# Optimization experiments

Measured on AMD Instinct MI355X. Metric: run time of the kernel, lower is better.

## Reference

```python
import jax, jax.numpy as jnp
import numpy as np

RADIUS = 8
NUM = 200
EPS = 1e-8


def _conv2d(x, k, pad_mode):
    # x: [B,1,H,W], k: [kh,kw]; same-size conv with given numpy-style padding mode
    ph, pw = k.shape[0] // 2, k.shape[1] // 2
    xp = jnp.pad(x, ((0, 0), (0, 0), (ph, ph), (pw, pw)), mode=pad_mode)
    return jax.lax.conv_general_dilated(
        xp, k[None, None], (1, 1), 'VALID',
        dimension_numbers=('NCHW', 'OIHW', 'NCHW'))


def _gauss_kernel7():
    xs = np.arange(7, dtype=np.float32) - 3.0
    g = np.exp(-0.5 * xs ** 2)
    g /= g.sum()
    return jnp.asarray(np.outer(g, g))


def get_corners(imgs):
    B, _, H, W = imgs.shape
    # kornia rgb_to_grayscale
    gray = 0.299 * imgs[:, 0:1] + 0.587 * imgs[:, 1:2] + 0.114 * imgs[:, 2:3]
    # kornia CornerGFTT: sobel gradients (normalized), gaussian-smoothed structure tensor, min eigenvalue
    sob = jnp.array([[-1., 0., 1.], [-2., 0., 2.], [-1., 0., 1.]], jnp.float32) / 8.0
    dx = _conv2d(gray, sob, 'edge')
    dy = _conv2d(gray, sob.T, 'edge')
    g = _gauss_kernel7()
    dx2 = _conv2d(dx * dx, g, 'reflect')
    dy2 = _conv2d(dy * dy, g, 'reflect')
    dxy = _conv2d(dx * dy, g, 'reflect')
    tr = dx2 + dy2
    det = dx2 * dy2 - dxy * dxy
    resp = 0.5 * (tr - jnp.sqrt(jnp.abs(tr * tr - 4.0 * det)))  # GFTT score (min eigval)
    # kornia nms2d with 5x5 window: keep local maxima
    mp = jax.lax.reduce_window(resp, -jnp.inf, jax.lax.max,
                               (1, 1, 5, 5), (1, 1, 1, 1),
                               [(0, 0), (0, 0), (2, 2), (2, 2)])
    resp = jnp.where(resp == mp, resp, 0.0)
    # unfold/mask/fold with kernel=stride=RADIUS == per non-overlapping 8x8 block:
    # keep elements equal to the block max and > 0
    r = RADIUS
    blk = resp.reshape(B, 1, H // r, r, W // r, r)
    bmax = blk.max(axis=(3, 5), keepdims=True)
    blk = jnp.where((blk > 0) & (blk == bmax), blk, 0.0)
    corners = blk.reshape(B, H * W)
    # top-200 scatter then binarize
    vals, idx = jax.lax.top_k(corners, NUM)
    out = jnp.zeros_like(corners).at[jnp.arange(B)[:, None], idx].set(vals)
    return (out > 0).astype(imgs.dtype).reshape(B, 1, H, W)


def setup_inputs() -> dict:
    key = jax.random.key(0)
    k1, k2, k3, k4 = jax.random.split(key, 4)
    B, N, D, H, W = 16, 2048, 256, 384, 384
    return {
        'descriptors': jax.random.normal(k1, (B, N, D), jnp.float32),
        'scores': jax.random.uniform(k2, (B, N), jnp.float32),
        'scores_dense': jax.random.normal(k3, (B, 1, H, W), jnp.float32),
        'imgs': jax.random.uniform(k4, (B, 3, H, W), jnp.float32),
    }


def reference(descriptors, scores, scores_dense, imgs):
    corners = get_corners(imgs)
    # all-pairs cosine similarity within each batch: pcos[b,i,j]
    norms = jnp.linalg.norm(descriptors, axis=-1)  # [B,N]
    dots = jnp.einsum('bnd,bmd->bnm', descriptors, descriptors)
    pcos = dots / jnp.maximum(norms[:, :, None] * norms[:, None, :], EPS)
    # BCEWithLogitsLoss(scores_dense, corners), mean reduction
    bce = jnp.mean(jnp.logaddexp(0.0, scores_dense) - scores_dense * corners)
    return bce + jnp.mean(jax.nn.relu(pcos))
```

## Files before the change

kernel.cpp:

```cpp
#include <hip/hip_runtime.h>

#define H 384
#define W 384
#define HWSZ (H * W)
#define NB 16
#define ND 2048
#define DD 256

#define OFF_RESP  256
#define OFF_CVAL  9437440
#define OFF_CPOS  9584896
#define OFF_DESCB 9732352
#define OFF_INV   26509568
#define OFF_PSOFT 26640640
#define OFF_PGEMM 26643200
#define OFF_PCORN 26652160

__device__ __forceinline__ int clampi(int v) { return v < 0 ? 0 : (v > 383 ? 383 : v); }
__device__ __forceinline__ int refl(int v) { return v < 0 ? -v : (v >= 384 ? 766 - v : v); }

__device__ __forceinline__ unsigned f2e4m3(float x) {
  float a = fabsf(x);
  unsigned s = (__float_as_uint(x) >> 31) << 7;
  if (a >= 448.f) return s | 0x7E;
  if (a < 0.015625f) {
    int m = (int)rintf(a * 512.f);
    return s | (unsigned)m;
  }
  unsigned u = __float_as_uint(a);
  u += 0x7FFFF + ((u >> 20) & 1);
  unsigned e = (u >> 23) - 120;
  unsigned m = (u >> 20) & 7;
  return s | (e << 3) | m;
}

typedef float f32x4 __attribute__((ext_vector_type(4)));

__device__ __forceinline__ void load_lds16(const void* g, void* l) {
  __builtin_amdgcn_global_load_lds((const __attribute__((address_space(1))) void*)g,
                                   (__attribute__((address_space(3))) void*)l, 16, 0, 0);
}

__global__ __launch_bounds__(256) void stage1_kernel(const float* __restrict__ imgs,
                                                     float* __restrict__ resp,
                                                     const float* __restrict__ desc,
                                                     unsigned char* __restrict__ descF8,
                                                     float* __restrict__ invn) {
  __shared__ float pbuf[4448];
  __shared__ float ubuf[3648];
  float* p0 = pbuf;
  float* p1 = pbuf + 1482;
  float* p2 = pbuf + 2964;
  float* glf = ubuf;
  float* t0 = ubuf;
  float* t1 = ubuf + 1216;
  float* t2 = ubuf + 2432;

  if (blockIdx.x >= 2304) {
    int wave = threadIdx.x >> 6, lane = threadIdx.x & 63;
    int row = (blockIdx.x - 2304) * 4 + wave;
    const float4* src = (const float4*)(desc + (size_t)row * DD);
    float4 v = src[lane];
    unsigned pk = f2e4m3(v.x) | (f2e4m3(v.y) << 8) | (f2e4m3(v.z) << 16) | (f2e4m3(v.w) << 24);
    ((unsigned*)(descF8 + (size_t)row * DD))[lane] = pk;
    float ss = v.x * v.x + v.y * v.y + v.z * v.z + v.w * v.w;
    for (int off = 32; off; off >>= 1) ss += __shfl_down(ss, off, 64);
    if (lane == 0) invn[row] = 1.f / fmaxf(sqrtf(ss), 1e-4f);
    return;
  }

  const float GW[7] = {0.0044330482f, 0.0540055826f, 0.2420362294f, 0.3990502160f,
                       0.2420362294f, 0.0540055826f, 0.0044330482f};
  int bid = blockIdx.x;
  int b = bid / 144;
  int t = bid % 144;
  int Y0 = (t / 12) * 32, X0 = (t % 12) * 32;
  const float* ib = imgs + (size_t)b * 3 * HWSZ;

  for (int i = threadIdx.x; i < 1600; i += 256) {
    int r = i / 40, c = i % 40;
    int gy = clampi(Y0 - 4 + r), gx = clampi(X0 - 4 + c);
    const float* p = ib + gy * W + gx;
    glf[r * 41 + c] = 0.299f * p[0] + 0.587f * p[HWSZ] + 0.114f * p[2 * HWSZ];
  }
  __syncthreads();

  bool interior = (X0 >= 32 && X0 <= 320 && Y0 >= 32 && Y0 <= 320);

  if (interior) {
    for (int i = threadIdx.x; i < 1444; i += 256) {
      int r = i / 38, c = i % 38;
      const float* g0 = glf + r * 41 + c;
      float a = g0[0],  bb = g0[1],  cc = g0[2];
      float d = g0[41],              e = g0[43];
      float f = g0[82], g = g0[83],  h = g0[84];
      float dx = 0.125f * ((cc - a) + 2.f * (e - d) + (h - f));
      float dy = 0.125f * ((f - a) + 2.f * (g - bb) + (h - cc));
      p0[r * 39 + c] = dx * dx;
      p1[r * 39 + c] = dy * dy;
      p2[r * 39 + c] = dx * dy;
    }
  } else {
    for (int i = threadIdx.x; i < 1444; i += 256) {
      int r = i / 38, c = i % 38;
      int py = refl(Y0 - 3 + r), px = refl(X0 - 3 + c);
      int ym = clampi(py - 1) - (Y0 - 4), y0 = py - (Y0 - 4), yp = clampi(py + 1) - (Y0 - 4);
      int xm = clampi(px - 1) - (X0 - 4), x0 = px - (X0 - 4), xp = clampi(px + 1) - (X0 - 4);
      float a = glf[ym * 41 + xm], bb = glf[ym * 41 + x0], cc = glf[ym * 41 + xp];
      float d = glf[y0 * 41 + xm], e = glf[y0 * 41 + xp];
      float f = glf[yp * 41 + xm], g = glf[yp * 41 + x0], h = glf[yp * 41 + xp];
      float dx = 0.125f * ((cc - a) + 2.f * (e - d) + (h - f));
      float dy = 0.125f * ((f - a) + 2.f * (g - bb) + (h - cc));
      p0[r * 39 + c] = dx * dx;
      p1[r * 39 + c] = dy * dy;
      p2[r * 39 + c] = dx * dy;
    }
  }
  __syncthreads();

  for (int g = threadIdx.x; g < 304; g += 256) {
    int r = g >> 3, c0 = (g & 7) * 4;
    {
      float a[10];
#pragma unroll
      for (int dc = 0; dc < 10; dc++) a[dc] = p0[r * 39 + c0 + dc];
#pragma unroll
      for (int k = 0; k < 4; k++) {
        float sv = 0.f;
#pragma unroll
        for (int j = 0; j < 7; j++) sv += GW[j] * a[k + j];
        t0[r * 32 + c0 + k] = sv;
      }
    }
    {
      float a[10];
#pragma unroll
      for (int dc = 0; dc < 10; dc++) a[dc] = p1[r * 39 + c0 + dc];
#pragma unroll
      for (int k = 0; k < 4; k++) {
        float sv = 0.f;
#pragma unroll
        for (int j = 0; j < 7; j++) sv += GW[j] * a[k + j];
        t1[r * 32 + c0 + k] = sv;
      }
    }
    {
      float a[10];
#pragma unroll
      for (int dc = 0; dc < 10; dc++) a[dc] = p2[r * 39 + c0 + dc];
#pragma unroll
      for (int k = 0; k < 4; k++) {
        float sv = 0.f;
#pragma unroll
        for (int j = 0; j < 7; j++) sv += GW[j] * a[k + j];
        t2[r * 32 + c0 + k] = sv;
      }
    }
  }
  __syncthreads();

  {
    int r0 = (threadIdx.x >> 5) * 4, c = threadIdx.x & 31;
    float s0[4], s1[4], s2[4];
    {
      float a[10];
#pragma unroll
      for (int dr = 0; dr < 10; dr++) a[dr] = t0[(r0 + dr) * 32 + c];
#pragma unroll
      for (int k = 0; k < 4; k++) {
        float sv = 0.f;
#pragma unroll
        for (int j = 0; j < 7; j++) sv += GW[j] * a[k + j];
        s0[k] = sv;
      }
    }
    {
      float a[10];
#pragma unroll
      for (int dr = 0; dr < 10; dr++) a[dr] = t1[(r0 + dr) * 32 + c];
#pragma unroll
      for (int k = 0; k < 4; k++) {
        float sv = 0.f;
#pragma unroll
        for (int j = 0; j < 7; j++) sv += GW[j] * a[k + j];
        s1[k] = sv;
      }
    }
    {
      float a[10];
#pragma unroll
      for (int dr = 0; dr < 10; dr++) a[dr] = t2[(r0 + dr) * 32 + c];
#pragma unroll
      for (int k = 0; k < 4; k++) {
        float sv = 0.f;
#pragma unroll
        for (int j = 0; j < 7; j++) sv += GW[j] * a[k + j];
        s2[k] = sv;
      }
    }
#pragma unroll
    for (int k = 0; k < 4; k++) {
      float tr = s0[k] + s1[k];
      float det = s0[k] * s1[k] - s2[k] * s2[k];
      float disc = tr * tr - 4.f * det;
      float rv = 0.5f * (tr - sqrtf(fabsf(disc)));
      resp[(size_t)b * HWSZ + (Y0 + r0 + k) * W + (X0 + c)] = rv;
    }
  }
}

__global__ __launch_bounds__(256) void stage2_kernel(const float* __restrict__ resp,
                                                     float* __restrict__ cval,
                                                     unsigned* __restrict__ cpos,
                                                     const float4* __restrict__ sd4,
                                                     float* __restrict__ psoft) {
  __shared__ float rl[68][37];
  __shared__ float rmx[68][32];
  __shared__ float r4[4];

  if (blockIdx.x >= 1152) {
    int sb = blockIdx.x - 1152;
    float s = 0.f;
    int base = sb * 256 + threadIdx.x;
#pragma unroll
    for (int it = 0; it < 4; it++) {
      float4 v = sd4[base + it * 147456];
      s += fmaxf(v.x, 0.f) + log1pf(expf(-fabsf(v.x))) +
           fmaxf(v.y, 0.f) + log1pf(expf(-fabsf(v.y))) +
           fmaxf(v.z, 0.f) + log1pf(expf(-fabsf(v.z))) +
           fmaxf(v.w, 0.f) + log1pf(expf(-fabsf(v.w)));
    }
    for (int off = 32; off; off >>= 1) s += __shfl_down(s, off, 64);
    if ((threadIdx.x & 63) == 0) r4[threadIdx.x >> 6] = s;
    __syncthreads();
    if (threadIdx.x == 0) psoft[sb] = r4[0] + r4[1] + r4[2] + r4[3];
    return;
  }

  int bid = blockIdx.x;
  int b = bid / 72;
  int t = bid % 72;
  int Y0 = (t / 12) * 64, X0 = (t % 12) * 32;
  const float* rb = resp + (size_t)b * HWSZ;

  for (int i = threadIdx.x; i < 68 * 36; i += 256) {
    int r = i / 36, c = i % 36;
    int gy = Y0 - 2 + r, gx = X0 - 2 + c;
    float v = -INFINITY;
    if (gy >= 0 && gy < H && gx >= 0 && gx < W) v = rb[gy * W + gx];
    rl[r][c] = v;
  }
  __syncthreads();

  for (int i = threadIdx.x; i < 68 * 32; i += 256) {
    int r = i / 32, c = i % 32;
    float m = rl[r][c];
    m = fmaxf(m, rl[r][c + 1]);
    m = fmaxf(m, rl[r][c + 2]);
    m = fmaxf(m, rl[r][c + 3]);
    m = fmaxf(m, rl[r][c + 4]);
    rmx[r][c] = m;
  }
  __syncthreads();

  for (int i = threadIdx.x; i < 2048; i += 256) {
    int r = i / 32, c = i % 32;
    float m = rmx[r][c];
    m = fmaxf(m, rmx[r + 1][c]);
    m = fmaxf(m, rmx[r + 2][c]);
    m = fmaxf(m, rmx[r + 3][c]);
    m = fmaxf(m, rmx[r + 4][c]);
    float v = rl[r + 2][c + 2];
    rl[r + 2][c + 2] = (v == m) ? v : 0.f;
  }
  __syncthreads();

  if (threadIdx.x < 32) {
    int bi = threadIdx.x >> 2, bj = threadIdx.x & 3;
    float bv = 0.f;
    unsigned bp = 0;
    for (int rr = 0; rr < 8; rr++)
      for (int cc = 0; cc < 8; cc++) {
        float v = rl[bi * 8 + rr + 2][bj * 8 + cc + 2];
        if (v > bv) { bv = v; bp = (unsigned)((Y0 + bi * 8 + rr) * W + (X0 + bj * 8 + cc)); }
      }
    int ci = b * 2304 + (Y0 / 8 + bi) * 48 + (X0 / 8 + bj);
    cval[ci] = bv;
    cpos[ci] = bp;
  }
}

__global__ __launch_bounds__(256) void stage3_kernel(const float* __restrict__ cval,
                                                     const unsigned* __restrict__ cpos,
                                                     const float* __restrict__ sd,
                                                     float* __restrict__ pcorn,
                                                     const unsigned char* __restrict__ descF8,
                                                     const float* __restrict__ invn,
                                                     float* __restrict__ pgemm) {
  alignas(16) __shared__ char smem[32768];
  int tid = threadIdx.x;

  if (blockIdx.x < 16) {
    int* hist = (int*)smem;
    int* pick = (int*)(smem + 1024);
    int* eqcnt = (int*)(smem + 1032);
    int* ri = (int*)(smem + 1040);
    unsigned* eqpos = (unsigned*)(smem + 1056);
    float* r4 = (float*)(smem + 2080);

    int b = blockIdx.x;
    int t = tid;
    int lane = t & 63;

    unsigned bits[9], pos[9];
#pragma unroll
    for (int q = 0; q < 9; q++) {
      int i = t + q * 256;
      unsigned vb = 0, p = 0;
      if (i < 2304) {
        float v = cval[b * 2304 + i];
        if (v > 0.f) { vb = __float_as_uint(v); p = cpos[b * 2304 + i]; }
      }
      bits[q] = vb; pos[q] = p;
    }

    int P = 0;
#pragma unroll
    for (int q = 0; q < 9; q++) P += (bits[q] != 0u);
    for (int off = 32; off; off >>= 1) P += __shfl_down(P, off, 64);
    if (lane == 0) ri[t >> 6] = P;
    __syncthreads();
    int Ptot = ri[0] + ri[1] + ri[2] + ri[3];
    if (Ptot == 0) { if (t == 0) pcorn[b] = 0.f; return; }
    int K = Ptot < 200 ? Ptot : 200;

    unsigned prefix = 0;
    int krem = K;
    for (int shift = 24; shift >= 0; shift -= 8) {
      hist[t] = 0;
      __syncthreads();
#pragma unroll
      for (int q = 0; q < 9; q++) {
        if (bits[q] != 0u &&
            (shift == 24 || (bits[q] >> (shift + 8)) == (prefix >> (shift + 8))))
          atomicAdd(&hist[(bits[q] >> shift) & 0xFF], 1);
      }
      __syncthreads();
      if (t < 64) {
        int h0 = hist[4 * t], h1 = hist[4 * t + 1], h2 = hist[4 * t + 2], h3 = hist[4 * t + 3];
        int tot = h0 + h1 + h2 + h3;
        int acc = tot;
        for (int d = 1; d < 64; d <<= 1) {
          int o = __shfl_down(acc, d, 64);
          if (t + d < 64) acc += o;
        }
        int excl = acc - tot;
        int G3 = excl, G2 = excl + h3, G1 = excl + h3 + h2, G0 = excl + h3 + h2 + h1;
        if (G0 < krem && G0 + h0 >= krem) { pick[0] = 4 * t;     pick[1] = G0; }
        if (G1 < krem && G1 + h1 >= krem) { pick[0] = 4 * t + 1; pick[1] = G1; }
        if (G2 < krem && G2 + h2 >= krem) { pick[0] = 4 * t + 2; pick[1] = G2; }
        if (G3 < krem && G3 + h3 >= krem) { pick[0] = 4 * t + 3; pick[1] = G3; }
      }
      __syncthreads();
      prefix |= ((unsigned)pick[0]) << shift;
      krem -= pick[1];
      __syncthreads();
    }

    if (t == 0) *eqcnt = 0;
    __syncthreads();
    float s = 0.f;
#pragma unroll
    for (int q = 0; q < 9; q++) {
      if (bits[q] > prefix) s += sd[(size_t)b * HWSZ + pos[q]];
      else if (bits[q] != 0u && bits[q] == prefix) {
        int idx = atomicAdd(eqcnt, 1);
        if (idx < 256) eqpos[idx] = pos[q];
      }
    }
    __syncthreads();
    int m = *eqcnt;
    if (m <= krem) {
      if (t < m) s += sd[(size_t)b * HWSZ + eqpos[t]];
    } else {
      int mm = m < 256 ? m : 256;
      if (t < mm) {
        unsigned p = eqpos[t];
        int rank = 0;
        for (int u = 0; u < mm; u++) rank += (eqpos[u] < p);
        if (rank < krem) s += sd[(size_t)b * HWSZ + p];
      }
    }
    for (int off = 32; off; off >>= 1) s += __shfl_down(s, off, 64);
    if (lane == 0) r4[t >> 6] = s;
    __syncthreads();
    if (t == 0) pcorn[b] = r4[0] + r4[1] + r4[2] + r4[3];
    return;
  }

  char* lA = smem;
  char* lB = smem + 16384;

  int bxl = blockIdx.x - 16;
  int bx = ((bxl & 7) * 272) + (bxl >> 3);
  int batch = bx / 136;
  int rem = bx % 136;
  int ti = 0, rowlen = 16;
  while (rem >= rowlen) { rem -= rowlen; rowlen--; ti++; }
  int tj = ti + rem;

  const unsigned char* Ab = descF8 + (size_t)batch * ND * DD;
  const float* inv = invn + batch * ND;
  int I0 = ti * 128, J0 = tj * 128;

  int wave = tid >> 6, lane = tid & 63;
  int rm = lane & 15, kq = lane >> 4;
  int wr = wave >> 1, wc = wave & 1;
  int lrow = lane >> 3;
  int lcolb = ((lane & 7) ^ lrow) << 4;
  int cx = rm & 7;

  f32x4 accf[4][4];
#pragma unroll
  for (int m = 0; m < 4; m++)
#pragma unroll
    for (int n = 0; n < 4; n++) accf[m][n] = (f32x4){0.f, 0.f, 0.f, 0.f};

  for (int k0 = 0; k0 < DD; k0 += 128) {
#pragma unroll
    for (int q = 0; q < 4; q++) {
      int chunk = wave * 4 + q;
      load_lds16(Ab + (size_t)(I0 + chunk * 8 + lrow) * DD + k0 + lcolb, lA + chunk * 1024);
      load_lds16(Ab + (size_t)(J0 + chunk * 8 + lrow) * DD + k0 + lcolb, lB + chunk * 1024);
    }
    __syncthreads();
#pragma unroll
    for (int kk = 0; kk < 128; kk += 32) {
      long af[4], bfr[4];
      int koff = kk + kq * 8;
      int pcol = ((((koff >> 4) ^ cx) << 4) | (koff & 8));
#pragma unroll
      for (int m = 0; m < 4; m++)
        af[m] = *reinterpret_cast<const long*>(lA + (wr * 64 + m * 16 + rm) * 128 + pcol);
#pragma unroll
      for (int n = 0; n < 4; n++)
        bfr[n] = *reinterpret_cast<const long*>(lB + (wc * 64 + n * 16 + rm) * 128 + pcol);
#pragma unroll
      for (int m = 0; m < 4; m++)
#pragma unroll
        for (int n = 0; n < 4; n++)
          accf[m][n] = __builtin_amdgcn_mfma_f32_16x16x32_fp8_fp8(af[m], bfr[n], accf[m][n], 0, 0, 0);
    }
    __syncthreads();
  }

  float wgt = (ti == tj) ? 1.f : 2.f;
  float invC[4];
#pragma unroll
  for (int n = 0; n < 4; n++) invC[n] = inv[J0 + wc * 64 + n * 16 + rm];
  float psum = 0.f;
#pragma unroll
  for (int m = 0; m < 4; m++) {
#pragma unroll
    for (int r = 0; r < 4; r++) {
      float invR = inv[I0 + wr * 64 + m * 16 + kq * 4 + r];
#pragma unroll
      for (int n = 0; n < 4; n++) psum += fmaxf(accf[m][n][r] * invR * invC[n], 0.f);
    }
  }
  psum *= wgt;
  for (int off = 32; off; off >>= 1) psum += __shfl_down(psum, off, 64);
  float* r4 = (float*)smem;
  if (lane == 0) r4[wave] = psum;
  __syncthreads();
  if (tid == 0) pgemm[bx] = r4[0] + r4[1] + r4[2] + r4[3];
}

__global__ __launch_bounds__(256) void finalize_kernel(const float* __restrict__ psoft,
                                                       const float* __restrict__ pcorn,
                                                       const float* __restrict__ pgemm,
                                                       float* __restrict__ out) {
  __shared__ float r4[4];
  float bce = 0.f;
  for (int i = threadIdx.x; i < 576; i += 256) bce += psoft[i];
  if (threadIdx.x < 16) bce -= pcorn[threadIdx.x];
  float g = 0.f;
  for (int i = threadIdx.x; i < 2176; i += 256) g += pgemm[i];
  float t = bce * (1.f / 2359296.f) + g * (1.f / 67108864.f);
  for (int off = 32; off; off >>= 1) t += __shfl_down(t, off, 64);
  if ((threadIdx.x & 63) == 0) r4[threadIdx.x >> 6] = t;
  __syncthreads();
  if (threadIdx.x == 0) out[0] = r4[0] + r4[1] + r4[2] + r4[3];
}

extern "C" void kernel_launch(void* const* d_in, const int* in_sizes, int n_in,
                              void* d_out, int out_size, void* d_ws, size_t ws_size,
                              hipStream_t stream) {
  (void)in_sizes; (void)n_in; (void)out_size; (void)ws_size;
  const float* desc = (const float*)d_in[0];
  const float* sd = (const float*)d_in[2];
  const float* imgs = (const float*)d_in[3];
  float* out = (float*)d_out;

  char* w = (char*)d_ws;
  float* resp = (float*)(w + OFF_RESP);
  float* cval = (float*)(w + OFF_CVAL);
  unsigned* cpos = (unsigned*)(w + OFF_CPOS);
  unsigned char* descF8 = (unsigned char*)(w + OFF_DESCB);
  float* invn = (float*)(w + OFF_INV);
  float* psoft = (float*)(w + OFF_PSOFT);
  float* pgemm = (float*)(w + OFF_PGEMM);
  float* pcorn = (float*)(w + OFF_PCORN);

  stage1_kernel<<<10496, 256, 0, stream>>>(imgs, resp, desc, descF8, invn);
  stage2_kernel<<<1728, 256, 0, stream>>>(resp, cval, cpos, (const float4*)sd, psoft);
  stage3_kernel<<<2192, 256, 0, stream>>>(cval, cpos, sd, pcorn, descF8, invn, pgemm);
  finalize_kernel<<<1, 256, 0, stream>>>(psoft, pcorn, pgemm, out);
}
```

Before: 153.4 us.

## Fold finalize into stage3 via atomic counters and coarsen descriptor conversion blocks

Removes the separate finalize kernel launch. Each GEMM block publishes its partial sum and bumps a global counter, and the last of the 16 corner blocks spin-waits until all GEMM blocks have arrived, then computes the final reduction inside stage3. Counters are reset in stage2. The descriptor FP8 conversion path in stage1 is also coarsened so each wave handles 8 rows, which cuts that grid from 8192 to 1024 blocks. The spin-wait depends on the GEMM blocks making forward progress while a corner block sits waiting, and this relies on relaxed atomics plus manual waitcnt for memory ordering.

```diff
diff --git a/kernel.cpp b/kernel.cpp
--- a/kernel.cpp
+++ b/kernel.cpp
@@ -15,6 +15,7 @@
 #define OFF_PSOFT 26640640
 #define OFF_PGEMM 26643200
 #define OFF_PCORN 26652160
+#define OFF_CNT   26652224
 
 __device__ __forceinline__ int clampi(int v) { return v < 0 ? 0 : (v > 383 ? 383 : v); }
 __device__ __forceinline__ int refl(int v) { return v < 0 ? -v : (v >= 384 ? 766 - v : v); }
@@ -39,6 +40,13 @@
 __device__ __forceinline__ void load_lds16(const void* g, void* l) {
   __builtin_amdgcn_global_load_lds((const __attribute__((address_space(1))) void*)g,
                                    (__attribute__((address_space(3))) void*)l, 16, 0, 0);
+}
+
+__device__ __forceinline__ void pubf(float* p, float v) {
+  __hip_atomic_store(p, v, __ATOMIC_RELAXED, __HIP_MEMORY_SCOPE_AGENT);
+}
+__device__ __forceinline__ float rdf(const float* p) {
+  return __hip_atomic_load(p, __ATOMIC_RELAXED, __HIP_MEMORY_SCOPE_AGENT);
 }
 
 __global__ __launch_bounds__(256) void stage1_kernel(const float* __restrict__ imgs,
@@ -58,14 +66,18 @@
 
   if (blockIdx.x >= 2304) {
     int wave = threadIdx.x >> 6, lane = threadIdx.x & 63;
-    int row = (blockIdx.x - 2304) * 4 + wave;
-    const float4* src = (const float4*)(desc + (size_t)row * DD);
-    float4 v = src[lane];
-    unsigned pk = f2e4m3(v.x) | (f2e4m3(v.y) << 8) | (f2e4m3(v.z) << 16) | (f2e4m3(v.w) << 24);
-    ((unsigned*)(descF8 + (size_t)row * DD))[lane] = pk;
-    float ss = v.x * v.x + v.y * v.y + v.z * v.z + v.w * v.w;
-    for (int off = 32; off; off >>= 1) ss += __shfl_down(ss, off, 64);
-    if (lane == 0) invn[row] = 1.f / fmaxf(sqrtf(ss), 1e-4f);
+    int rbase = (blockIdx.x - 2304) * 32 + wave * 8;
+#pragma unroll 2
+    for (int it = 0; it < 8; it++) {
+      int row = rbase + it;
+      const float4* src = (const float4*)(desc + (size_t)row * DD);
+      float4 v = src[lane];
+      unsigned pk = f2e4m3(v.x) | (f2e4m3(v.y) << 8) | (f2e4m3(v.z) << 16) | (f2e4m3(v.w) << 24);
+      ((unsigned*)(descF8 + (size_t)row * DD))[lane] = pk;
+      float ss = v.x * v.x + v.y * v.y + v.z * v.z + v.w * v.w;
+      for (int off = 32; off; off >>= 1) ss += __shfl_down(ss, off, 64);
+      if (lane == 0) invn[row] = 1.f / fmaxf(sqrtf(ss), 1e-4f);
+    }
     return;
   }
 
@@ -213,13 +225,15 @@
                                                      float* __restrict__ cval,
                                                      unsigned* __restrict__ cpos,
                                                      const float4* __restrict__ sd4,
-                                                     float* __restrict__ psoft) {
+                                                     float* __restrict__ psoft,
+                                                     int* __restrict__ cnt) {
   __shared__ float rl[68][37];
   __shared__ float rmx[68][32];
   __shared__ float r4[4];
 
   if (blockIdx.x >= 1152) {
     int sb = blockIdx.x - 1152;
+    if (sb == 0 && threadIdx.x == 0) { cnt[0] = 0; cnt[1] = 0; }
     float s = 0.f;
     int base = sb * 256 + threadIdx.x;
 #pragma unroll
@@ -296,8 +310,12 @@
                                                      float* __restrict__ pcorn,
                                                      const unsigned char* __restrict__ descF8,
                                                      const float* __restrict__ invn,
-                                                     float* __restrict__ pgemm) {
+                                                     float* __restrict__ pgemm,
+                                                     const float* __restrict__ psoft,
+                                                     int* __restrict__ cnt,
+                                                     float* __restrict__ out) {
   alignas(16) __shared__ char smem[32768];
+  __shared__ int finFlag;
   int tid = threadIdx.x;
 
   if (blockIdx.x < 16) {
@@ -331,70 +349,97 @@
     if (lane == 0) ri[t >> 6] = P;
     __syncthreads();
     int Ptot = ri[0] + ri[1] + ri[2] + ri[3];
-    if (Ptot == 0) { if (t == 0) pcorn[b] = 0.f; return; }
-    int K = Ptot < 200 ? Ptot : 200;
-
-    unsigned prefix = 0;
-    int krem = K;
-    for (int shift = 24; shift >= 0; shift -= 8) {
-      hist[t] = 0;
+
+    float total = 0.f;
+    if (Ptot > 0) {
+      int K = Ptot < 200 ? Ptot : 200;
+
+      unsigned prefix = 0;
+      int krem = K;
+      for (int shift = 24; shift >= 0; shift -= 8) {
+        hist[t] = 0;
+        __syncthreads();
+#pragma unroll
+        for (int q = 0; q < 9; q++) {
+          if (bits[q] != 0u &&
+              (shift == 24 || (bits[q] >> (shift + 8)) == (prefix >> (shift + 8))))
+            atomicAdd(&hist[(bits[q] >> shift) & 0xFF], 1);
+        }
+        __syncthreads();
+        if (t < 64) {
+          int h0 = hist[4 * t], h1 = hist[4 * t + 1], h2 = hist[4 * t + 2], h3 = hist[4 * t + 3];
+          int tot = h0 + h1 + h2 + h3;
+          int acc = tot;
+          for (int d = 1; d < 64; d <<= 1) {
+            int o = __shfl_down(acc, d, 64);
+            if (t + d < 64) acc += o;
+          }
+          int excl = acc - tot;
+          int G3 = excl, G2 = excl + h3, G1 = excl + h3 + h2, G0 = excl + h3 + h2 + h1;
+          if (G0 < krem && G0 + h0 >= krem) { pick[0] = 4 * t;     pick[1] = G0; }
+          if (G1 < krem && G1 + h1 >= krem) { pick[0] = 4 * t + 1; pick[1] = G1; }
+          if (G2 < krem && G2 + h2 >= krem) { pick[0] = 4 * t + 2; pick[1] = G2; }
+          if (G3 < krem && G3 + h3 >= krem) { pick[0] = 4 * t + 3; pick[1] = G3; }
+        }
+        __syncthreads();
+        prefix |= ((unsigned)pick[0]) << shift;
+        krem -= pick[1];
+        __syncthreads();
+      }
+
+      if (t == 0) *eqcnt = 0;
       __syncthreads();
+      float s = 0.f;
 #pragma unroll
       for (int q = 0; q < 9; q++) {
-        if (bits[q] != 0u &&
-            (shift == 24 || (bits[q] >> (shift + 8)) == (prefix >> (shift + 8))))
-          atomicAdd(&hist[(bits[q] >> shift) & 0xFF], 1);
+        if (bits[q] > prefix) s += sd[(size_t)b * HWSZ + pos[q]];
+        else if (bits[q] != 0u && bits[q] == prefix) {
+          int idx = atomicAdd(eqcnt, 1);
+          if (idx < 256) eqpos[idx] = pos[q];
+        }
       }
       __syncthreads();
-      if (t < 64) {
-        int h0 = hist[4 * t], h1 = hist[4 * t + 1], h2 = hist[4 * t + 2], h3 = hist[4 * t + 3];
-        int tot = h0 + h1 + h2 + h3;
-        int acc = tot;
-        for (int d = 1; d < 64; d <<= 1) {
-          int o = __shfl_down(acc, d, 64);
-          if (t + d < 64) acc += o;
+      int m = *eqcnt;
+      if (m <= krem) {
+        if (t < m) s += sd[(size_t)b * HWSZ + eqpos[t]];
+      } else {
+        int mm = m < 256 ? m : 256;
+        if (t < mm) {
+          unsigned p = eqpos[t];
+          int rank = 0;
+          for (int u = 0; u < mm; u++) rank += (eqpos[u] < p);
+          if (rank < krem) s += sd[(size_t)b * HWSZ + p];
         }
-        int excl = acc - tot;
-        int G3 = excl, G2 = excl + h3, G1 = excl + h3 + h2, G0 = excl + h3 + h2 + h1;
-        if (G0 < krem && G0 + h0 >= krem) { pick[0] = 4 * t;     pick[1] = G0; }
-        if (G1 < krem && G1 + h1 >= krem) { pick[0] = 4 * t + 1; pick[1] = G1; }
-        if (G2 < krem && G2 + h2 >= krem) { pick[0] = 4 * t + 2; pick[1] = G2; }
-        if (G3 < krem && G3 + h3 >= krem) { pick[0] = 4 * t + 3; pick[1] = G3; }
-      }
+      }
+      for (int off = 32; off; off >>= 1) s += __shfl_down(s, off, 64);
+      if (lane == 0) r4[t >> 6] = s;
       __syncthreads();
-      prefix |= ((unsigned)pick[0]) << shift;
-      krem -= pick[1];
-      __syncthreads();
-    }
-
-    if (t == 0) *eqcnt = 0;
+      total = r4[0] + r4[1] + r4[2] + r4[3];
+    }
+
+    if (t == 0) {
+      pubf(&pcorn[b], total);
+      asm volatile("s_waitcnt vmcnt(0)" ::: "memory");
+      int arr = __hip_atomic_fetch_add(&cnt[1], 1, __ATOMIC_RELAXED, __HIP_MEMORY_SCOPE_AGENT);
+      finFlag = (arr == 15);
+      if (finFlag) {
+        while (__hip_atomic_load(&cnt[0], __ATOMIC_RELAXED, __HIP_MEMORY_SCOPE_AGENT) < 2176)
+          __builtin_amdgcn_s_sleep(16);
+      }
+    }
     __syncthreads();
-    float s = 0.f;
-#pragma unroll
-    for (int q = 0; q < 9; q++) {
-      if (bits[q] > prefix) s += sd[(size_t)b * HWSZ + pos[q]];
-      else if (bits[q] != 0u && bits[q] == prefix) {
-        int idx = atomicAdd(eqcnt, 1);
-        if (idx < 256) eqpos[idx] = pos[q];
-      }
-    }
+    if (!finFlag) return;
+
+    float bce = 0.f;
+    for (int i = t; i < 576; i += 256) bce += psoft[i];
+    if (t < 16) bce -= rdf(&pcorn[t]);
+    float g = 0.f;
+    for (int i = t; i < 2176; i += 256) g += rdf(&pgemm[i]);
+    float v = bce * (1.f / 2359296.f) + g * (1.f / 67108864.f);
+    for (int off = 32; off; off >>= 1) v += __shfl_down(v, off, 64);
+    if (lane == 0) r4[t >> 6] = v;
     __syncthreads();
-    int m = *eqcnt;
-    if (m <= krem) {
-      if (t < m) s += sd[(size_t)b * HWSZ + eqpos[t]];
-    } else {
-      int mm = m < 256 ? m : 256;
-      if (t < mm) {
-        unsigned p = eqpos[t];
-        int rank = 0;
-        for (int u = 0; u < mm; u++) rank += (eqpos[u] < p);
-        if (rank < krem) s += sd[(size_t)b * HWSZ + p];
-      }
-    }
-    for (int off = 32; off; off >>= 1) s += __shfl_down(s, off, 64);
-    if (lane == 0) r4[t >> 6] = s;
-    __syncthreads();
-    if (t == 0) pcorn[b] = r4[0] + r4[1] + r4[2] + r4[3];
+    if (t == 0) out[0] = r4[0] + r4[1] + r4[2] + r4[3];
     return;
   }
 
@@ -473,24 +518,11 @@
   float* r4 = (float*)smem;
   if (lane == 0) r4[wave] = psum;
   __syncthreads();
-  if (tid == 0) pgemm[bx] = r4[0] + r4[1] + r4[2] + r4[3];
-}
-
-__global__ __launch_bounds__(256) void finalize_kernel(const float* __restrict__ psoft,
-                                                       const float* __restrict__ pcorn,
-                                                       const float* __restrict__ pgemm,
-                                                       float* __restrict__ out) {
-  __shared__ float r4[4];
-  float bce = 0.f;
-  for (int i = threadIdx.x; i < 576; i += 256) bce += psoft[i];
-  if (threadIdx.x < 16) bce -= pcorn[threadIdx.x];
-  float g = 0.f;
-  for (int i = threadIdx.x; i < 2176; i += 256) g += pgemm[i];
-  float t = bce * (1.f / 2359296.f) + g * (1.f / 67108864.f);
-  for (int off = 32; off; off >>= 1) t += __shfl_down(t, off, 64);
-  if ((threadIdx.x & 63) == 0) r4[threadIdx.x >> 6] = t;
-  __syncthreads();
-  if (threadIdx.x == 0) out[0] = r4[0] + r4[1] + r4[2] + r4[3];
+  if (tid == 0) {
+    pubf(&pgemm[bx], r4[0] + r4[1] + r4[2] + r4[3]);
+    asm volatile("s_waitcnt vmcnt(0)" ::: "memory");
+    __hip_atomic_fetch_add(&cnt[0], 1, __ATOMIC_RELAXED, __HIP_MEMORY_SCOPE_AGENT);
+  }
 }
 
 extern "C" void kernel_launch(void* const* d_in, const int* in_sizes, int n_in,
@@ -511,9 +543,10 @@
   float* psoft = (float*)(w + OFF_PSOFT);
   float* pgemm = (float*)(w + OFF_PGEMM);
   float* pcorn = (float*)(w + OFF_PCORN);
-
-  stage1_kernel<<<10496, 256, 0, stream>>>(imgs, resp, desc, descF8, invn);
-  stage2_kernel<<<1728, 256, 0, stream>>>(resp, cval, cpos, (const float4*)sd, psoft);
-  stage3_kernel<<<2192, 256, 0, stream>>>(cval, cpos, sd, pcorn, descF8, invn, pgemm);
-  finalize_kernel<<<1, 256, 0, stream>>>(psoft, pcorn, pgemm, out);
-}
+  int* cnt = (int*)(w + OFF_CNT);
+
+  stage1_kernel<<<3328, 256, 0, stream>>>(imgs, resp, desc, descF8, invn);
+  stage2_kernel<<<1728, 256, 0, stream>>>(resp, cval, cpos, (const float4*)sd, psoft, cnt);
+  stage3_kernel<<<2192, 256, 0, stream>>>(cval, cpos, sd, pcorn, descF8, invn,
+                                          pgemm, psoft, cnt, out);
+}
```

Measured after the change: 169.4 us. 1.1x slower.
